# Kernel tuning notes

Hardware: AMD Instinct MI355X
Metric: run time of the kernel (lower is better)

Reference implementation:

```python
import jax, jax.numpy as jnp
import numpy as np

H = 2048      # hidden_size
NH = 32       # num attention heads
KVH = 8       # num kv heads
HD = 64       # head_dim
G = NH // KVH # kv groups (4)
EPS = 1e-6
THETA = 1000000.0


def _rms_norm(x, g):
    # normalize over last dim (head_dim)
    var = jnp.mean(jnp.square(x), axis=-1, keepdims=True)
    return x * jax.lax.rsqrt(var + EPS) * g


def _rope(seq_len, dtype):
    inv_freq = 1.0 / (THETA ** (jnp.arange(0, HD, 2, dtype=jnp.float32) / HD))
    pos = jnp.arange(seq_len, dtype=jnp.float32)
    freqs = pos[:, None] * inv_freq[None, :]          # [S, HD/2]
    emb = jnp.concatenate([freqs, freqs], axis=-1)    # [S, HD]
    return jnp.cos(emb).astype(dtype), jnp.sin(emb).astype(dtype)


def _rotate_half(x):
    x1, x2 = jnp.split(x, 2, axis=-1)
    return jnp.concatenate([-x2, x1], axis=-1)


def setup_inputs() -> dict:
    key = jax.random.key(0)
    ks = jax.random.split(key, 8)
    B, S = 1, 2048
    s = lambda fan_in: 1.0 / np.sqrt(fan_in)
    return {
        "hidden_states": jax.random.normal(ks[0], (B, S, H), jnp.float32),
        "Wq": jax.random.normal(ks[1], (H, NH * HD + NH), jnp.float32) * s(H),
        "Wk": jax.random.normal(ks[2], (H, KVH * HD), jnp.float32) * s(H),
        "Wv": jax.random.normal(ks[3], (H, KVH * HD), jnp.float32) * s(H),
        "Wo": jax.random.normal(ks[4], (NH * HD, H), jnp.float32) * s(NH * HD),
        "g_q": jnp.ones((HD,), jnp.float32),
        "g_k": jnp.ones((HD,), jnp.float32),
    }


def reference(hidden_states, Wq, Wk, Wv, Wo, g_q, g_k):
    B, S, _ = hidden_states.shape
    dtype = hidden_states.dtype

    qg = hidden_states @ Wq                              # [B,S,NH*HD+NH]
    k = hidden_states @ Wk                               # [B,S,KVH*HD]
    v = hidden_states @ Wv

    # headwise gate split, grouped per kv head (matches torch view/split)
    qg = qg.reshape(B, S, KVH, G * HD + G)
    q, gate = qg[..., : G * HD], qg[..., G * HD :]       # gate: [B,S,KVH,G]
    gate = gate.reshape(B, S, NH, 1)
    q = q.reshape(B, S, NH, HD).transpose(0, 2, 1, 3)    # [B,NH,S,HD]
    k = k.reshape(B, S, KVH, HD).transpose(0, 2, 1, 3)   # [B,KVH,S,HD]
    v = v.reshape(B, S, KVH, HD).transpose(0, 2, 1, 3)

    q = _rms_norm(q, g_q)
    k = _rms_norm(k, g_k)

    cos, sin = _rope(S, dtype)                           # [S,HD]
    cos, sin = cos[None, None], sin[None, None]
    q = q * cos + _rotate_half(q) * sin
    k = k * cos + _rotate_half(k) * sin

    # GQA: repeat kv heads
    k = jnp.repeat(k, G, axis=1)                         # [B,NH,S,HD]
    v = jnp.repeat(v, G, axis=1)

    # causal SDPA
    scale = 1.0 / np.sqrt(HD)
    scores = jnp.einsum("bhqd,bhkd->bhqk", q, k) * scale
    causal = jnp.tril(jnp.ones((S, S), bool))
    scores = jnp.where(causal[None, None], scores, jnp.finfo(dtype).min)
    probs = jax.nn.softmax(scores, axis=-1)
    attn = jnp.einsum("bhqk,bhkd->bhqd", probs, v)       # [B,NH,S,HD]

    attn = attn.transpose(0, 2, 1, 3)                    # [B,S,NH,HD]
    attn = attn * jax.nn.sigmoid(gate)
    attn = attn.reshape(B, S, NH * HD)
    return attn @ Wo
```

## Files before the change

### kernel.cpp

```cpp
#include <hip/hip_runtime.h>
#include <hip/hip_bf16.h>

#define SLEN 2048
#define HDIM 2048
#define NHEAD 32
#define KVHEAD 8
#define HEADD 64
#define NTOT 3104
#define NPAD 3200

typedef short bh8 __attribute__((ext_vector_type(8)));
typedef float f32x4 __attribute__((ext_vector_type(4)));

#define QSCALE 0.1803368801111204f

__device__ __forceinline__ unsigned short f2bf(float f) {
    union { float f; unsigned int u; } v; v.f = f;
    unsigned int u = v.u;
    return (unsigned short)((u + 0x7fffu + ((u >> 16) & 1u)) >> 16);
}

__device__ __forceinline__ unsigned int cvtpk_bf16(float lo, float hi) {
    unsigned int r;
    asm("v_cvt_pk_bf16_f32 %0, %1, %2" : "=v"(r) : "v"(lo), "v"(hi));
    return r;
}

__device__ __forceinline__ void gl_lds16(const unsigned short* g, unsigned short* l) {
    __builtin_amdgcn_global_load_lds(
        (const __attribute__((address_space(1))) unsigned int*)g,
        (__attribute__((address_space(3))) unsigned int*)l, 16, 0, 0);
}

__global__ void cast_x_k(const float* __restrict__ src, unsigned short* __restrict__ dst, int n) {
    int i = blockIdx.x * blockDim.x + threadIdx.x;
    int base = i * 4;
    if (base < n) {
        float4 f = *(const float4*)(src + base);
        ushort4 o;
        o.x = f2bf(f.x); o.y = f2bf(f.y); o.z = f2bf(f.z); o.w = f2bf(f.w);
        *(ushort4*)(dst + base) = o;
    }
}

__global__ void pack_wt_k(const float* __restrict__ Wq, const float* __restrict__ Wk,
                          const float* __restrict__ Wv, unsigned short* __restrict__ Wt) {
    __shared__ float tile[32][33];
    int n0 = blockIdx.x * 32, k0 = blockIdx.y * 32;
    int t = threadIdx.x;
    for (int i = 0; i < 4; i++) {
        int idx = i * 256 + t;
        int kr = idx >> 5, nc = idx & 31;
        int n = n0 + nc, k = k0 + kr;
        float val = 0.f;
        if (n < 2048)       { int h = n >> 6, d = n & 63; val = Wq[(size_t)k * 2080 + (h >> 2) * 260 + (h & 3) * 64 + d]; }
        else if (n < 2080)  { int h = n - 2048;           val = Wq[(size_t)k * 2080 + (h >> 2) * 260 + 256 + (h & 3)]; }
        else if (n < 2592)  { val = Wk[(size_t)k * 512 + (n - 2080)]; }
        else if (n < 3104)  { val = Wv[(size_t)k * 512 + (n - 2592)]; }
        tile[kr][nc] = val;
    }
    __syncthreads();
    for (int i = 0; i < 4; i++) {
        int idx = i * 256 + t;
        int nr = idx >> 5, kc = idx & 31;
        Wt[(size_t)(n0 + nr) * HDIM + (k0 + kc)] = f2bf(tile[kc][nr]);
    }
}

__global__ void pack_wot_k(const float* __restrict__ Wo, unsigned short* __restrict__ Wt) {
    __shared__ float tile[32][33];
    int n0 = blockIdx.x * 32, k0 = blockIdx.y * 32;
    int t = threadIdx.x;
    for (int i = 0; i < 4; i++) {
        int idx = i * 256 + t;
        int kr = idx >> 5, nc = idx & 31;
        tile[kr][nc] = Wo[(size_t)(k0 + kr) * 2048 + (n0 + nc)];
    }
    __syncthreads();
    for (int i = 0; i < 4; i++) {
        int idx = i * 256 + t;
        int nr = idx >> 5, kc = idx & 31;
        Wt[(size_t)(n0 + nr) * 2048 + (k0 + kc)] = f2bf(tile[kc][nr]);
    }
}

__global__ __launch_bounds__(256) void gemm_nt_k(const unsigned short* __restrict__ A,
                                                 const unsigned short* __restrict__ Bt,
                                                 float* __restrict__ C,
                                                 int K, int ldc) {
    __shared__ unsigned short As[3][128 * 32];
    __shared__ unsigned short Bs[3][128 * 32];
    int d = blockIdx.y * gridDim.x + blockIdx.x;
    int nwg = gridDim.x * gridDim.y;
    int cpx = nwg >> 3;
    int swz = (d & 7) * cpx + (d >> 3);
    int m0 = (swz % gridDim.x) * 128, n0 = (swz / gridDim.x) * 128;
    int t = threadIdx.x;
    int w = t >> 6, l = t & 63;
    int wm = (w >> 1) * 64, wn = (w & 1) * 64;
    int lrow = l & 15, lc = l >> 4;
    int rsw = (lrow >> 1) & 3;
    int srowA = w * 32 + (l >> 2);
    int scol = ((l & 3) ^ ((l >> 3) & 3)) * 8;

    f32x4 acc[4][4];
    #pragma unroll
    for (int i = 0; i < 4; i++)
        #pragma unroll
        for (int j = 0; j < 4; j++)
            acc[i][j] = {0.f, 0.f, 0.f, 0.f};

    const unsigned short* ga = &A[(size_t)(m0 + srowA) * K + scol];
    const unsigned short* gb = &Bt[(size_t)(n0 + srowA) * K + scol];
    int nst = K >> 5;

#define STAGE_NT(s, b) do { \
        const unsigned short* ga0 = ga + (size_t)(s) * 32; \
        const unsigned short* gb0 = gb + (size_t)(s) * 32; \
        gl_lds16(ga0,                  &As[b][(w * 2 + 0) * 512]); \
        gl_lds16(ga0 + 16 * (size_t)K, &As[b][(w * 2 + 1) * 512]); \
        gl_lds16(gb0,                  &Bs[b][(w * 2 + 0) * 512]); \
        gl_lds16(gb0 + 16 * (size_t)K, &Bs[b][(w * 2 + 1) * 512]); \
    } while (0)

    STAGE_NT(0, 0);
    STAGE_NT(1, 1);
    int rd = 0, wr = 2;
    for (int s = 0; s < nst; s++) {
        if (s + 1 < nst) asm volatile("s_waitcnt vmcnt(4)\n\ts_barrier" ::: "memory");
        else             asm volatile("s_waitcnt vmcnt(0)\n\ts_barrier" ::: "memory");
        if (s + 2 < nst) STAGE_NT(s + 2, wr);
        bh8 af[4], bb[4];
        #pragma unroll
        for (int i = 0; i < 4; i++) {
            af[i] = *(const bh8*)(&As[rd][(wm + i * 16 + lrow) * 32 + ((lc ^ rsw) * 8)]);
            bb[i] = *(const bh8*)(&Bs[rd][(wn + i * 16 + lrow) * 32 + ((lc ^ rsw) * 8)]);
        }
        #pragma unroll
        for (int i = 0; i < 4; i++)
            #pragma unroll
            for (int j = 0; j < 4; j++)
                acc[i][j] = __builtin_amdgcn_mfma_f32_16x16x32_bf16(af[i], bb[j], acc[i][j], 0, 0, 0);
        rd = (rd == 2) ? 0 : rd + 1;
        wr = (wr == 2) ? 0 : wr + 1;
    }
#undef STAGE_NT
    int col = l & 15, rbase = (l >> 4) * 4;
    for (int i = 0; i < 4; i++)
        for (int j = 0; j < 4; j++)
            #pragma unroll
            for (int r = 0; r < 4; r++)
                C[(size_t)(m0 + wm + i * 16 + rbase + r) * ldc + (n0 + wn + j * 16 + col)] = acc[i][j][r];
}

__global__ __launch_bounds__(256) void gemm_nt64_k(const unsigned short* __restrict__ A,
                                                   const unsigned short* __restrict__ Bt,
                                                   float* __restrict__ C) {
    const int K = 2048, ldc = 2048;
    __shared__ unsigned short As[3][64 * 32];
    __shared__ unsigned short Bs[3][128 * 32];
    int d = blockIdx.x;
    int swz = (d & 7) * 64 + (d >> 3);
    int m0 = (swz & 31) * 64, n0 = (swz >> 5) * 128;
    int t = threadIdx.x;
    int w = t >> 6, l = t & 63;
    int wm = (w >> 1) * 32, wn = (w & 1) * 64;
    int lrow = l & 15, lc = l >> 4;
    int rsw = (lrow >> 1) & 3;
    int scol = ((l & 3) ^ ((l >> 3) & 3)) * 8;

    f32x4 acc[2][4];
    #pragma unroll
    for (int i = 0; i < 2; i++)
        #pragma unroll
        for (int j = 0; j < 4; j++)
            acc[i][j] = {0.f, 0.f, 0.f, 0.f};

    const unsigned short* ga = &A[(size_t)(m0 + w * 16 + (l >> 2)) * K + scol];
    const unsigned short* gb = &Bt[(size_t)(n0 + w * 32 + (l >> 2)) * K + scol];
    const int nst = K >> 5;

#define STAGE_NT64(s, b) do { \
        gl_lds16(ga + (size_t)(s) * 32,                  &As[b][w * 512]); \
        gl_lds16(gb + (size_t)(s) * 32,                  &Bs[b][(w * 2 + 0) * 512]); \
        gl_lds16(gb + (size_t)(s) * 32 + 16 * (size_t)K, &Bs[b][(w * 2 + 1) * 512]); \
    } while (0)

    STAGE_NT64(0, 0);
    STAGE_NT64(1, 1);
    int rd = 0, wr = 2;
    for (int s = 0; s < nst; s++) {
        if (s + 1 < nst) asm volatile("s_waitcnt vmcnt(3)\n\ts_barrier" ::: "memory");
        else             asm volatile("s_waitcnt vmcnt(0)\n\ts_barrier" ::: "memory");
        if (s + 2 < nst) STAGE_NT64(s + 2, wr);
        bh8 af[2], bb[4];
        #pragma unroll
        for (int i = 0; i < 2; i++)
            af[i] = *(const bh8*)(&As[rd][(wm + i * 16 + lrow) * 32 + ((lc ^ rsw) * 8)]);
        #pragma unroll
        for (int j = 0; j < 4; j++)
            bb[j] = *(const bh8*)(&Bs[rd][(wn + j * 16 + lrow) * 32 + ((lc ^ rsw) * 8)]);
        #pragma unroll
        for (int i = 0; i < 2; i++)
            #pragma unroll
            for (int j = 0; j < 4; j++)
                acc[i][j] = __builtin_amdgcn_mfma_f32_16x16x32_bf16(af[i], bb[j], acc[i][j], 0, 0, 0);
        rd = (rd == 2) ? 0 : rd + 1;
        wr = (wr == 2) ? 0 : wr + 1;
    }
#undef STAGE_NT64
    int col = l & 15, rbase = (l >> 4) * 4;
    for (int i = 0; i < 2; i++)
        for (int j = 0; j < 4; j++)
            #pragma unroll
            for (int r = 0; r < 4; r++)
                C[(size_t)(m0 + wm + i * 16 + rbase + r) * ldc + (n0 + wn + j * 16 + col)] = acc[i][j][r];
}

__global__ void norm_rope_k(const float* __restrict__ QKVG, unsigned short* __restrict__ Qr,
                            unsigned short* __restrict__ Kr,
                            const float* __restrict__ g_q, const float* __restrict__ g_k) {
    int wid = blockIdx.x * (blockDim.x >> 6) + (threadIdx.x >> 6);
    int lane = threadIdx.x & 63;
    int type, s, hh;
    if (wid < SLEN * NHEAD) { type = 0; s = wid >> 5; hh = wid & 31; }
    else                    { int r = wid - SLEN * NHEAD; type = 1; s = r >> 3; hh = r & 7; }
    int col = (type == 0) ? hh * 64 + lane : 2080 + hh * 64 + lane;
    float x = QKVG[(size_t)s * NPAD + col];
    float sq = x * x;
    #pragma unroll
    for (int off = 32; off; off >>= 1) sq += __shfl_xor(sq, off);
    float inv = rsqrtf(sq * (1.f / 64.f) + 1e-6f);
    float g = (type == 0 ? g_q : g_k)[lane];
    float xn = x * inv * g;
    float xp = __shfl_xor(xn, 32);
    float xr = (lane < 32) ? -xp : xp;
    int i = lane & 31;
    float invf = __expf(-(float)i * (0.03125f * 13.815510557964274f));
    float ang = (float)s * invf;
    float c = cosf(ang), sn = sinf(ang);
    float r = xn * c + xr * sn;
    if (type == 0) Qr[((size_t)hh * SLEN + s) * 64 + lane] = f2bf(r * QSCALE);
    else           Kr[((size_t)hh * SLEN + s) * 64 + lane] = f2bf(r);
}

__global__ void vt_k(const float* __restrict__ QKVG, unsigned short* __restrict__ Vt) {
    __shared__ float tile[64][65];
    int s0 = blockIdx.x * 64, hh = blockIdx.y;
    int t = threadIdx.x;
    #pragma unroll
    for (int i = 0; i < 4; i++) {
        int idx = i * 256 + t;
        int sr = idx >> 4, c4 = (idx & 15) * 4;
        float4 f = *(const float4*)(&QKVG[(size_t)(s0 + sr) * NPAD + 2592 + hh * 64 + c4]);
        tile[sr][c4] = f.x; tile[sr][c4 + 1] = f.y; tile[sr][c4 + 2] = f.z; tile[sr][c4 + 3] = f.w;
    }
    __syncthreads();
    #pragma unroll
    for (int i = 0; i < 4; i++) {
        int idx = i * 256 + t;
        int dr = idx >> 4, c4 = (idx & 15) * 4;
        int hb = c4 >> 5, f = (c4 >> 4) & 1, g = (c4 >> 2) & 3;
        int p = (hb * 4 + g) * 8 + f * 4;
        ushort4 o;
        o.x = f2bf(tile[c4][dr]); o.y = f2bf(tile[c4 + 1][dr]);
        o.z = f2bf(tile[c4 + 2][dr]); o.w = f2bf(tile[c4 + 3][dr]);
        *(ushort4*)(&Vt[((size_t)hh * 64 + dr) * SLEN + s0 + p]) = o;
    }
}

__global__ void gate_sig_k(const float* __restrict__ QKVG, float* __restrict__ gate) {
    int i = blockIdx.x * 256 + threadIdx.x;
    int s = i >> 5, h = i & 31;
    float x = QKVG[(size_t)s * NPAD + 2048 + h];
    gate[i] = 1.f / (1.f + __expf(-x));
}

__global__ __launch_bounds__(256) void attn_k(const unsigned short* __restrict__ Qr,
                                              const unsigned short* __restrict__ Kr,
                                              const unsigned short* __restrict__ Vt,
                                              const float* __restrict__ gate,
                                              unsigned short* __restrict__ attn) {
    __shared__ unsigned short Kls[3][64 * 64];
    __shared__ unsigned short Vls[3][64 * 64];
    int d = blockIdx.y * gridDim.x + blockIdx.x;
    int kvh = d & 7;
    int j8 = d >> 3;
    int h = kvh * 4 + (j8 >> 4);
    int xp = j8 & 15;
    int t = threadIdx.x, w = t >> 6, l = t & 63;
    int ql = l & 15, g = l >> 4;
    const float NEGINF = -__builtin_inff();

    const unsigned short* Kh = Kr + (size_t)kvh * SLEN * 64;
    const unsigned short* Vh = Vt + (size_t)kvh * 64 * SLEN;
    const unsigned short* Qh = Qr + (size_t)h * SLEN * 64;
    int lk = g * 8;
    int r8 = l >> 3, c8 = l & 7;
    int cs = 8 * (c8 ^ r8);
    int R0 = w * 16, R1 = w * 16 + 8;
    int rdswz = (ql & 7) << 4;

    for (int half = 0; half < 2; half++) {
        int qt = half ? 31 - xp : xp;
        int q0 = qt * 64;
        int qrow = q0 + w * 16 + ql;

        bh8 qa0 = *(const bh8*)(Qh + (size_t)qrow * 64 + lk);
        bh8 qa1 = *(const bh8*)(Qh + (size_t)qrow * 64 + 32 + lk);

        f32x4 o[4];
        #pragma unroll
        for (int i = 0; i < 4; i++) o[i] = {0.f, 0.f, 0.f, 0.f};
        float m2 = NEGINF, lsum = 0.f;

        int ntiles = qt + 1;
        {
            gl_lds16(&Kh[(size_t)(0 + R0 + r8) * 64 + cs], &Kls[0][R0 * 64]);
            gl_lds16(&Kh[(size_t)(0 + R1 + r8) * 64 + cs], &Kls[0][R1 * 64]);
            gl_lds16(&Vh[(size_t)(R0 + r8) * SLEN + 0 + cs], &Vls[0][R0 * 64]);
            gl_lds16(&Vh[(size_t)(R1 + r8) * SLEN + 0 + cs], &Vls[0][R1 * 64]);
        }
        if (ntiles > 1) {
            gl_lds16(&Kh[(size_t)(64 + R0 + r8) * 64 + cs], &Kls[1][R0 * 64]);
            gl_lds16(&Kh[(size_t)(64 + R1 + r8) * 64 + cs], &Kls[1][R1 * 64]);
            gl_lds16(&Vh[(size_t)(R0 + r8) * SLEN + 64 + cs], &Vls[1][R0 * 64]);
            gl_lds16(&Vh[(size_t)(R1 + r8) * SLEN + 64 + cs], &Vls[1][R1 * 64]);
        }
        int rd = 0, wr = 2;

        for (int ti = 0; ti < ntiles; ti++) {
            if (ti + 1 < ntiles) asm volatile("s_waitcnt vmcnt(4)\n\ts_barrier" ::: "memory");
            else                 asm volatile("s_waitcnt vmcnt(0)\n\ts_barrier" ::: "memory");
            if (ti + 2 < ntiles) {
                int kv1 = (ti + 2) * 64;
                gl_lds16(&Kh[(size_t)(kv1 + R0 + r8) * 64 + cs], &Kls[wr][R0 * 64]);
                gl_lds16(&Kh[(size_t)(kv1 + R1 + r8) * 64 + cs], &Kls[wr][R1 * 64]);
                gl_lds16(&Vh[(size_t)(R0 + r8) * SLEN + kv1 + cs], &Vls[wr][R0 * 64]);
                gl_lds16(&Vh[(size_t)(R1 + r8) * SLEN + kv1 + cs], &Vls[wr][R1 * 64]);
            }
            const unsigned short* Kb = &Kls[rd][0];
            const unsigned short* Vb = &Vls[rd][0];
            int kv0 = ti * 64;
            f32x4 sct[4];
            #pragma unroll
            for (int nt = 0; nt < 4; nt++) {
                int rb = (nt * 16 + ql) * 128;
                bh8 kb0 = *(const bh8*)(&Kb[(rb + ((g * 16) ^ rdswz)) >> 1]);
                bh8 kb1 = *(const bh8*)(&Kb[(rb + ((64 + g * 16) ^ rdswz)) >> 1]);
                f32x4 a = {0.f, 0.f, 0.f, 0.f};
                a = __builtin_amdgcn_mfma_f32_16x16x32_bf16(kb0, qa0, a, 0, 0, 0);
                a = __builtin_amdgcn_mfma_f32_16x16x32_bf16(kb1, qa1, a, 0, 0, 0);
                sct[nt] = a;
            }
            if (ti == qt) {
                #pragma unroll
                for (int nt = 0; nt < 4; nt++)
                    #pragma unroll
                    for (int j = 0; j < 4; j++) {
                        int key = kv0 + nt * 16 + 4 * g + j;
                        if (key > qrow) sct[nt][j] = NEGINF;
                    }
            }
            float mt0 = fmaxf(fmaxf(sct[0][0], sct[0][1]), fmaxf(sct[0][2], sct[0][3]));
            float mt1 = fmaxf(fmaxf(sct[1][0], sct[1][1]), fmaxf(sct[1][2], sct[1][3]));
            float mt2 = fmaxf(fmaxf(sct[2][0], sct[2][1]), fmaxf(sct[2][2], sct[2][3]));
            float mt3 = fmaxf(fmaxf(sct[3][0], sct[3][1]), fmaxf(sct[3][2], sct[3][3]));
            float mt = fmaxf(fmaxf(mt0, mt1), fmaxf(mt2, mt3));
            mt = fmaxf(mt, __shfl_xor(mt, 16));
            mt = fmaxf(mt, __shfl_xor(mt, 32));
            if (!__all(mt - m2 <= 8.f)) {
                float mnew = fmaxf(m2, mt);
                float resc = __builtin_amdgcn_exp2f(m2 - mnew);
                m2 = mnew;
                lsum *= resc;
                float rf[4];
                #pragma unroll
                for (int j = 0; j < 4; j++) rf[j] = __shfl(resc, 4 * g + j);
                #pragma unroll
                for (int nt = 0; nt < 4; nt++) {
                    f32x4 oo = o[nt];
                    #pragma unroll
                    for (int j = 0; j < 4; j++) oo[j] *= rf[j];
                    o[nt] = oo;
                }
            }
            float ps = 0.f;
            #pragma unroll
            for (int nt = 0; nt < 4; nt++)
                #pragma unroll
                for (int j = 0; j < 4; j++) {
                    float p = __builtin_amdgcn_exp2f(sct[nt][j] - m2);
                    sct[nt][j] = p;
                    ps += p;
                }
            ps += __shfl_xor(ps, 16);
            ps += __shfl_xor(ps, 32);
            lsum += ps;
            union { unsigned int u[4]; bh8 v; } pa0, pa1;
            pa0.u[0] = cvtpk_bf16(sct[0][0], sct[0][1]);
            pa0.u[1] = cvtpk_bf16(sct[0][2], sct[0][3]);
            pa0.u[2] = cvtpk_bf16(sct[1][0], sct[1][1]);
            pa0.u[3] = cvtpk_bf16(sct[1][2], sct[1][3]);
            pa1.u[0] = cvtpk_bf16(sct[2][0], sct[2][1]);
            pa1.u[1] = cvtpk_bf16(sct[2][2], sct[2][3]);
            pa1.u[2] = cvtpk_bf16(sct[3][0], sct[3][1]);
            pa1.u[3] = cvtpk_bf16(sct[3][2], sct[3][3]);
            #pragma unroll
            for (int nt = 0; nt < 4; nt++) {
                int rb = (nt * 16 + ql) * 128;
                bh8 vb0 = *(const bh8*)(&Vb[(rb + ((g * 16) ^ rdswz)) >> 1]);
                bh8 vb1 = *(const bh8*)(&Vb[(rb + ((64 + g * 16) ^ rdswz)) >> 1]);
                o[nt] = __builtin_amdgcn_mfma_f32_16x16x32_bf16(pa0.v, vb0, o[nt], 0, 0, 0);
                o[nt] = __builtin_amdgcn_mfma_f32_16x16x32_bf16(pa1.v, vb1, o[nt], 0, 0, 0);
            }
            rd = (rd == 2) ? 0 : rd + 1;
            wr = (wr == 2) ? 0 : wr + 1;
        }
        asm volatile("s_barrier" ::: "memory");

        float gf[4];
        #pragma unroll
        for (int j = 0; j < 4; j++) {
            float ls = __shfl(lsum, 4 * g + j);
            int row = q0 + w * 16 + 4 * g + j;
            gf[j] = gate[row * 32 + h] / ls;
        }
        #pragma unroll
        for (int j = 0; j < 4; j++) {
            int row = q0 + w * 16 + 4 * g + j;
            #pragma unroll
            for (int nt = 0; nt < 4; nt++)
                attn[(size_t)row * 2048 + h * 64 + nt * 16 + ql] = f2bf(o[nt][j] * gf[j]);
        }
    }
}

extern "C" void kernel_launch(void* const* d_in, const int* in_sizes, int n_in,
                              void* d_out, int out_size, void* d_ws, size_t ws_size,
                              hipStream_t stream) {
    const float* hidden = (const float*)d_in[0];
    const float* Wq = (const float*)d_in[1];
    const float* Wk = (const float*)d_in[2];
    const float* Wv = (const float*)d_in[3];
    const float* Wo = (const float*)d_in[4];
    const float* gq = (const float*)d_in[5];
    const float* gk = (const float*)d_in[6];
    float* out = (float*)d_out;
    char* ws = (char*)d_ws;

    unsigned short* X    = (unsigned short*)(ws + 0);
    unsigned short* Wt   = (unsigned short*)(ws + 8388608);
    float*          QKVG = (float*)(ws + 21495808);
    unsigned short* Qr   = (unsigned short*)(ws + 47710208);
    unsigned short* Kr   = (unsigned short*)(ws + 56098816);
    unsigned short* Vt   = (unsigned short*)(ws + 58195968);
    float*          gate = (float*)(ws + 60293120);
    unsigned short* attn = (unsigned short*)(ws + 60555264);
    unsigned short* Wot  = (unsigned short*)(ws + 68943872);

    cast_x_k<<<dim3(4096), dim3(256), 0, stream>>>(hidden, X, SLEN * HDIM);
    pack_wt_k<<<dim3(100, 64), dim3(256), 0, stream>>>(Wq, Wk, Wv, Wt);
    pack_wot_k<<<dim3(64, 64), dim3(256), 0, stream>>>(Wo, Wot);
    gemm_nt_k<<<dim3(16, 25), dim3(256), 0, stream>>>(X, Wt, QKVG, HDIM, NPAD);
    norm_rope_k<<<dim3(20480), dim3(256), 0, stream>>>(QKVG, Qr, Kr, gq, gk);
    vt_k<<<dim3(32, 8), dim3(256), 0, stream>>>(QKVG, Vt);
    gate_sig_k<<<dim3(256), dim3(256), 0, stream>>>(QKVG, gate);
    attn_k<<<dim3(16, 32), dim3(256), 0, stream>>>(Qr, Kr, Vt, gate, attn);
    gemm_nt64_k<<<dim3(512), dim3(256), 0, stream>>>(attn, Wot, out);
}
```

Measured before the change: 170.1 us.

## Reuse 64x128 GEMM for QKV projection, split attention blocks, add MFMA priority

The QKV projection now uses the 64x128-tile GEMM kernel with a generic swizzle (800 workgroups) instead of the 128x128 kernel, giving more workgroups to fill the CUs. The attention kernel drops its paired-half causal balancing and launches one workgroup per (head, q-tile), ordered longest-first, over 1024 blocks. s_setprio is raised around MFMA sections in both the GEMM and attention kernels to favour matrix work among co-resident waves. The risks are lower per-block data reuse in the smaller GEMM tile and load imbalance in the tail of the attention grid.

```diff
diff --git a/kernel.cpp b/kernel.cpp
--- a/kernel.cpp
+++ b/kernel.cpp
@@ -84,84 +84,18 @@
     }
 }
 
-__global__ __launch_bounds__(256) void gemm_nt_k(const unsigned short* __restrict__ A,
-                                                 const unsigned short* __restrict__ Bt,
-                                                 float* __restrict__ C,
-                                                 int K, int ldc) {
-    __shared__ unsigned short As[3][128 * 32];
-    __shared__ unsigned short Bs[3][128 * 32];
-    int d = blockIdx.y * gridDim.x + blockIdx.x;
-    int nwg = gridDim.x * gridDim.y;
-    int cpx = nwg >> 3;
-    int swz = (d & 7) * cpx + (d >> 3);
-    int m0 = (swz % gridDim.x) * 128, n0 = (swz / gridDim.x) * 128;
-    int t = threadIdx.x;
-    int w = t >> 6, l = t & 63;
-    int wm = (w >> 1) * 64, wn = (w & 1) * 64;
-    int lrow = l & 15, lc = l >> 4;
-    int rsw = (lrow >> 1) & 3;
-    int srowA = w * 32 + (l >> 2);
-    int scol = ((l & 3) ^ ((l >> 3) & 3)) * 8;
-
-    f32x4 acc[4][4];
-    #pragma unroll
-    for (int i = 0; i < 4; i++)
-        #pragma unroll
-        for (int j = 0; j < 4; j++)
-            acc[i][j] = {0.f, 0.f, 0.f, 0.f};
-
-    const unsigned short* ga = &A[(size_t)(m0 + srowA) * K + scol];
-    const unsigned short* gb = &Bt[(size_t)(n0 + srowA) * K + scol];
-    int nst = K >> 5;
-
-#define STAGE_NT(s, b) do { \
-        const unsigned short* ga0 = ga + (size_t)(s) * 32; \
-        const unsigned short* gb0 = gb + (size_t)(s) * 32; \
-        gl_lds16(ga0,                  &As[b][(w * 2 + 0) * 512]); \
-        gl_lds16(ga0 + 16 * (size_t)K, &As[b][(w * 2 + 1) * 512]); \
-        gl_lds16(gb0,                  &Bs[b][(w * 2 + 0) * 512]); \
-        gl_lds16(gb0 + 16 * (size_t)K, &Bs[b][(w * 2 + 1) * 512]); \
-    } while (0)
-
-    STAGE_NT(0, 0);
-    STAGE_NT(1, 1);
-    int rd = 0, wr = 2;
-    for (int s = 0; s < nst; s++) {
-        if (s + 1 < nst) asm volatile("s_waitcnt vmcnt(4)\n\ts_barrier" ::: "memory");
-        else             asm volatile("s_waitcnt vmcnt(0)\n\ts_barrier" ::: "memory");
-        if (s + 2 < nst) STAGE_NT(s + 2, wr);
-        bh8 af[4], bb[4];
-        #pragma unroll
-        for (int i = 0; i < 4; i++) {
-            af[i] = *(const bh8*)(&As[rd][(wm + i * 16 + lrow) * 32 + ((lc ^ rsw) * 8)]);
-            bb[i] = *(const bh8*)(&Bs[rd][(wn + i * 16 + lrow) * 32 + ((lc ^ rsw) * 8)]);
-        }
-        #pragma unroll
-        for (int i = 0; i < 4; i++)
-            #pragma unroll
-            for (int j = 0; j < 4; j++)
-                acc[i][j] = __builtin_amdgcn_mfma_f32_16x16x32_bf16(af[i], bb[j], acc[i][j], 0, 0, 0);
-        rd = (rd == 2) ? 0 : rd + 1;
-        wr = (wr == 2) ? 0 : wr + 1;
-    }
-#undef STAGE_NT
-    int col = l & 15, rbase = (l >> 4) * 4;
-    for (int i = 0; i < 4; i++)
-        for (int j = 0; j < 4; j++)
-            #pragma unroll
-            for (int r = 0; r < 4; r++)
-                C[(size_t)(m0 + wm + i * 16 + rbase + r) * ldc + (n0 + wn + j * 16 + col)] = acc[i][j][r];
-}
-
 __global__ __launch_bounds__(256) void gemm_nt64_k(const unsigned short* __restrict__ A,
                                                    const unsigned short* __restrict__ Bt,
-                                                   float* __restrict__ C) {
-    const int K = 2048, ldc = 2048;
+                                                   float* __restrict__ C,
+                                                   int ldc, int mtiles) {
+    const int K = 2048;
     __shared__ unsigned short As[3][64 * 32];
     __shared__ unsigned short Bs[3][128 * 32];
     int d = blockIdx.x;
-    int swz = (d & 7) * 64 + (d >> 3);
-    int m0 = (swz & 31) * 64, n0 = (swz >> 5) * 128;
+    int nwg = gridDim.x;
+    int cpx = nwg >> 3;
+    int swz = (d & 7) * cpx + (d >> 3);
+    int m0 = (swz % mtiles) * 64, n0 = (swz / mtiles) * 128;
     int t = threadIdx.x;
     int w = t >> 6, l = t & 63;
     int wm = (w >> 1) * 32, wn = (w & 1) * 64;
@@ -200,11 +134,13 @@
         #pragma unroll
         for (int j = 0; j < 4; j++)
             bb[j] = *(const bh8*)(&Bs[rd][(wn + j * 16 + lrow) * 32 + ((lc ^ rsw) * 8)]);
+        __builtin_amdgcn_s_setprio(1);
         #pragma unroll
         for (int i = 0; i < 2; i++)
             #pragma unroll
             for (int j = 0; j < 4; j++)
                 acc[i][j] = __builtin_amdgcn_mfma_f32_16x16x32_bf16(af[i], bb[j], acc[i][j], 0, 0, 0);
+        __builtin_amdgcn_s_setprio(0);
         rd = (rd == 2) ? 0 : rd + 1;
         wr = (wr == 2) ? 0 : wr + 1;
     }
@@ -283,11 +219,10 @@
                                               unsigned short* __restrict__ attn) {
     __shared__ unsigned short Kls[3][64 * 64];
     __shared__ unsigned short Vls[3][64 * 64];
-    int d = blockIdx.y * gridDim.x + blockIdx.x;
+    int d = blockIdx.x;
     int kvh = d & 7;
-    int j8 = d >> 3;
-    int h = kvh * 4 + (j8 >> 4);
-    int xp = j8 & 15;
+    int h = kvh * 4 + ((d >> 3) & 3);
+    int qt = 31 - (d >> 5);
     int t = threadIdx.x, w = t >> 6, l = t & 63;
     int ql = l & 15, g = l >> 4;
     const float NEGINF = -__builtin_inff();
@@ -301,138 +236,138 @@
     int R0 = w * 16, R1 = w * 16 + 8;
     int rdswz = (ql & 7) << 4;
 
-    for (int half = 0; half < 2; half++) {
-        int qt = half ? 31 - xp : xp;
-        int q0 = qt * 64;
-        int qrow = q0 + w * 16 + ql;
-
-        bh8 qa0 = *(const bh8*)(Qh + (size_t)qrow * 64 + lk);
-        bh8 qa1 = *(const bh8*)(Qh + (size_t)qrow * 64 + 32 + lk);
-
-        f32x4 o[4];
-        #pragma unroll
-        for (int i = 0; i < 4; i++) o[i] = {0.f, 0.f, 0.f, 0.f};
-        float m2 = NEGINF, lsum = 0.f;
-
-        int ntiles = qt + 1;
-        {
-            gl_lds16(&Kh[(size_t)(0 + R0 + r8) * 64 + cs], &Kls[0][R0 * 64]);
-            gl_lds16(&Kh[(size_t)(0 + R1 + r8) * 64 + cs], &Kls[0][R1 * 64]);
-            gl_lds16(&Vh[(size_t)(R0 + r8) * SLEN + 0 + cs], &Vls[0][R0 * 64]);
-            gl_lds16(&Vh[(size_t)(R1 + r8) * SLEN + 0 + cs], &Vls[0][R1 * 64]);
+    int q0 = qt * 64;
+    int qrow = q0 + w * 16 + ql;
+
+    bh8 qa0 = *(const bh8*)(Qh + (size_t)qrow * 64 + lk);
+    bh8 qa1 = *(const bh8*)(Qh + (size_t)qrow * 64 + 32 + lk);
+
+    f32x4 o[4];
+    #pragma unroll
+    for (int i = 0; i < 4; i++) o[i] = {0.f, 0.f, 0.f, 0.f};
+    float m2 = NEGINF, lsum = 0.f;
+
+    int ntiles = qt + 1;
+    {
+        gl_lds16(&Kh[(size_t)(0 + R0 + r8) * 64 + cs], &Kls[0][R0 * 64]);
+        gl_lds16(&Kh[(size_t)(0 + R1 + r8) * 64 + cs], &Kls[0][R1 * 64]);
+        gl_lds16(&Vh[(size_t)(R0 + r8) * SLEN + 0 + cs], &Vls[0][R0 * 64]);
+        gl_lds16(&Vh[(size_t)(R1 + r8) * SLEN + 0 + cs], &Vls[0][R1 * 64]);
+    }
+    if (ntiles > 1) {
+        gl_lds16(&Kh[(size_t)(64 + R0 + r8) * 64 + cs], &Kls[1][R0 * 64]);
+        gl_lds16(&Kh[(size_t)(64 + R1 + r8) * 64 + cs], &Kls[1][R1 * 64]);
+        gl_lds16(&Vh[(size_t)(R0 + r8) * SLEN + 64 + cs], &Vls[1][R0 * 64]);
+        gl_lds16(&Vh[(size_t)(R1 + r8) * SLEN + 64 + cs], &Vls[1][R1 * 64]);
+    }
+    int rd = 0, wr = 2;
+
+    for (int ti = 0; ti < ntiles; ti++) {
+        if (ti + 1 < ntiles) asm volatile("s_waitcnt vmcnt(4)\n\ts_barrier" ::: "memory");
+        else                 asm volatile("s_waitcnt vmcnt(0)\n\ts_barrier" ::: "memory");
+        if (ti + 2 < ntiles) {
+            int kv1 = (ti + 2) * 64;
+            gl_lds16(&Kh[(size_t)(kv1 + R0 + r8) * 64 + cs], &Kls[wr][R0 * 64]);
+            gl_lds16(&Kh[(size_t)(kv1 + R1 + r8) * 64 + cs], &Kls[wr][R1 * 64]);
+            gl_lds16(&Vh[(size_t)(R0 + r8) * SLEN + kv1 + cs], &Vls[wr][R0 * 64]);
+            gl_lds16(&Vh[(size_t)(R1 + r8) * SLEN + kv1 + cs], &Vls[wr][R1 * 64]);
         }
-        if (ntiles > 1) {
-            gl_lds16(&Kh[(size_t)(64 + R0 + r8) * 64 + cs], &Kls[1][R0 * 64]);
-            gl_lds16(&Kh[(size_t)(64 + R1 + r8) * 64 + cs], &Kls[1][R1 * 64]);
-            gl_lds16(&Vh[(size_t)(R0 + r8) * SLEN + 64 + cs], &Vls[1][R0 * 64]);
-            gl_lds16(&Vh[(size_t)(R1 + r8) * SLEN + 64 + cs], &Vls[1][R1 * 64]);
+        const unsigned short* Kb = &Kls[rd][0];
+        const unsigned short* Vb = &Vls[rd][0];
+        int kv0 = ti * 64;
+        f32x4 sct[4];
+        __builtin_amdgcn_s_setprio(1);
+        #pragma unroll
+        for (int nt = 0; nt < 4; nt++) {
+            int rb = (nt * 16 + ql) * 128;
+            bh8 kb0 = *(const bh8*)(&Kb[(rb + ((g * 16) ^ rdswz)) >> 1]);
+            bh8 kb1 = *(const bh8*)(&Kb[(rb + ((64 + g * 16) ^ rdswz)) >> 1]);
+            f32x4 a = {0.f, 0.f, 0.f, 0.f};
+            a = __builtin_amdgcn_mfma_f32_16x16x32_bf16(kb0, qa0, a, 0, 0, 0);
+            a = __builtin_amdgcn_mfma_f32_16x16x32_bf16(kb1, qa1, a, 0, 0, 0);
+            sct[nt] = a;
         }
-        int rd = 0, wr = 2;
-
-        for (int ti = 0; ti < ntiles; ti++) {
-            if (ti + 1 < ntiles) asm volatile("s_waitcnt vmcnt(4)\n\ts_barrier" ::: "memory");
-            else                 asm volatile("s_waitcnt vmcnt(0)\n\ts_barrier" ::: "memory");
-            if (ti + 2 < ntiles) {
-                int kv1 = (ti + 2) * 64;
-                gl_lds16(&Kh[(size_t)(kv1 + R0 + r8) * 64 + cs], &Kls[wr][R0 * 64]);
-                gl_lds16(&Kh[(size_t)(kv1 + R1 + r8) * 64 + cs], &Kls[wr][R1 * 64]);
-                gl_lds16(&Vh[(size_t)(R0 + r8) * SLEN + kv1 + cs], &Vls[wr][R0 * 64]);
-                gl_lds16(&Vh[(size_t)(R1 + r8) * SLEN + kv1 + cs], &Vls[wr][R1 * 64]);
-            }
-            const unsigned short* Kb = &Kls[rd][0];
-            const unsigned short* Vb = &Vls[rd][0];
-            int kv0 = ti * 64;
-            f32x4 sct[4];
-            #pragma unroll
-            for (int nt = 0; nt < 4; nt++) {
-                int rb = (nt * 16 + ql) * 128;
-                bh8 kb0 = *(const bh8*)(&Kb[(rb + ((g * 16) ^ rdswz)) >> 1]);
-                bh8 kb1 = *(const bh8*)(&Kb[(rb + ((64 + g * 16) ^ rdswz)) >> 1]);
-                f32x4 a = {0.f, 0.f, 0.f, 0.f};
-                a = __builtin_amdgcn_mfma_f32_16x16x32_bf16(kb0, qa0, a, 0, 0, 0);
-                a = __builtin_amdgcn_mfma_f32_16x16x32_bf16(kb1, qa1, a, 0, 0, 0);
-                sct[nt] = a;
-            }
-            if (ti == qt) {
-                #pragma unroll
-                for (int nt = 0; nt < 4; nt++)
-                    #pragma unroll
-                    for (int j = 0; j < 4; j++) {
-                        int key = kv0 + nt * 16 + 4 * g + j;
-                        if (key > qrow) sct[nt][j] = NEGINF;
-                    }
-            }
-            float mt0 = fmaxf(fmaxf(sct[0][0], sct[0][1]), fmaxf(sct[0][2], sct[0][3]));
-            float mt1 = fmaxf(fmaxf(sct[1][0], sct[1][1]), fmaxf(sct[1][2], sct[1][3]));
-            float mt2 = fmaxf(fmaxf(sct[2][0], sct[2][1]), fmaxf(sct[2][2], sct[2][3]));
-            float mt3 = fmaxf(fmaxf(sct[3][0], sct[3][1]), fmaxf(sct[3][2], sct[3][3]));
-            float mt = fmaxf(fmaxf(mt0, mt1), fmaxf(mt2, mt3));
-            mt = fmaxf(mt, __shfl_xor(mt, 16));
-            mt = fmaxf(mt, __shfl_xor(mt, 32));
-            if (!__all(mt - m2 <= 8.f)) {
-                float mnew = fmaxf(m2, mt);
-                float resc = __builtin_amdgcn_exp2f(m2 - mnew);
-                m2 = mnew;
-                lsum *= resc;
-                float rf[4];
-                #pragma unroll
-                for (int j = 0; j < 4; j++) rf[j] = __shfl(resc, 4 * g + j);
-                #pragma unroll
-                for (int nt = 0; nt < 4; nt++) {
-                    f32x4 oo = o[nt];
-                    #pragma unroll
-                    for (int j = 0; j < 4; j++) oo[j] *= rf[j];
-                    o[nt] = oo;
-                }
-            }
-            float ps = 0.f;
+        __builtin_amdgcn_s_setprio(0);
+        if (ti == qt) {
             #pragma unroll
             for (int nt = 0; nt < 4; nt++)
                 #pragma unroll
                 for (int j = 0; j < 4; j++) {
-                    float p = __builtin_amdgcn_exp2f(sct[nt][j] - m2);
-                    sct[nt][j] = p;
-                    ps += p;
+                    int key = kv0 + nt * 16 + 4 * g + j;
+                    if (key > qrow) sct[nt][j] = NEGINF;
                 }
-            ps += __shfl_xor(ps, 16);
-            ps += __shfl_xor(ps, 32);
-            lsum += ps;
-            union { unsigned int u[4]; bh8 v; } pa0, pa1;
-            pa0.u[0] = cvtpk_bf16(sct[0][0], sct[0][1]);
-            pa0.u[1] = cvtpk_bf16(sct[0][2], sct[0][3]);
-            pa0.u[2] = cvtpk_bf16(sct[1][0], sct[1][1]);
-            pa0.u[3] = cvtpk_bf16(sct[1][2], sct[1][3]);
-            pa1.u[0] = cvtpk_bf16(sct[2][0], sct[2][1]);
-            pa1.u[1] = cvtpk_bf16(sct[2][2], sct[2][3]);
-            pa1.u[2] = cvtpk_bf16(sct[3][0], sct[3][1]);
-            pa1.u[3] = cvtpk_bf16(sct[3][2], sct[3][3]);
+        }
+        float mt0 = fmaxf(fmaxf(sct[0][0], sct[0][1]), fmaxf(sct[0][2], sct[0][3]));
+        float mt1 = fmaxf(fmaxf(sct[1][0], sct[1][1]), fmaxf(sct[1][2], sct[1][3]));
+        float mt2 = fmaxf(fmaxf(sct[2][0], sct[2][1]), fmaxf(sct[2][2], sct[2][3]));
+        float mt3 = fmaxf(fmaxf(sct[3][0], sct[3][1]), fmaxf(sct[3][2], sct[3][3]));
+        float mt = fmaxf(fmaxf(mt0, mt1), fmaxf(mt2, mt3));
+        mt = fmaxf(mt, __shfl_xor(mt, 16));
+        mt = fmaxf(mt, __shfl_xor(mt, 32));
+        if (!__all(mt - m2 <= 8.f)) {
+            float mnew = fmaxf(m2, mt);
+            float resc = __builtin_amdgcn_exp2f(m2 - mnew);
+            m2 = mnew;
+            lsum *= resc;
+            float rf[4];
+            #pragma unroll
+            for (int j = 0; j < 4; j++) rf[j] = __shfl(resc, 4 * g + j);
             #pragma unroll
             for (int nt = 0; nt < 4; nt++) {
-                int rb = (nt * 16 + ql) * 128;
-                bh8 vb0 = *(const bh8*)(&Vb[(rb + ((g * 16) ^ rdswz)) >> 1]);
-                bh8 vb1 = *(const bh8*)(&Vb[(rb + ((64 + g * 16) ^ rdswz)) >> 1]);
-                o[nt] = __builtin_amdgcn_mfma_f32_16x16x32_bf16(pa0.v, vb0, o[nt], 0, 0, 0);
-                o[nt] = __builtin_amdgcn_mfma_f32_16x16x32_bf16(pa1.v, vb1, o[nt], 0, 0, 0);
+                f32x4 oo = o[nt];
+                #pragma unroll
+                for (int j = 0; j < 4; j++) oo[j] *= rf[j];
+                o[nt] = oo;
             }
-            rd = (rd == 2) ? 0 : rd + 1;
-            wr = (wr == 2) ? 0 : wr + 1;
         }
-        asm volatile("s_barrier" ::: "memory");
-
-        float gf[4];
-        #pragma unroll
-        for (int j = 0; j < 4; j++) {
-            float ls = __shfl(lsum, 4 * g + j);
-            int row = q0 + w * 16 + 4 * g + j;
-            gf[j] = gate[row * 32 + h] / ls;
+        float ps = 0.f;
+        #pragma unroll
+        for (int nt = 0; nt < 4; nt++)
+            #pragma unroll
+            for (int j = 0; j < 4; j++) {
+                float p = __builtin_amdgcn_exp2f(sct[nt][j] - m2);
+                sct[nt][j] = p;
+                ps += p;
+            }
+        ps += __shfl_xor(ps, 16);
+        ps += __shfl_xor(ps, 32);
+        lsum += ps;
+        union { unsigned int u[4]; bh8 v; } pa0, pa1;
+        pa0.u[0] = cvtpk_bf16(sct[0][0], sct[0][1]);
+        pa0.u[1] = cvtpk_bf16(sct[0][2], sct[0][3]);
+        pa0.u[2] = cvtpk_bf16(sct[1][0], sct[1][1]);
+        pa0.u[3] = cvtpk_bf16(sct[1][2], sct[1][3]);
+        pa1.u[0] = cvtpk_bf16(sct[2][0], sct[2][1]);
+        pa1.u[1] = cvtpk_bf16(sct[2][2], sct[2][3]);
+        pa1.u[2] = cvtpk_bf16(sct[3][0], sct[3][1]);
+        pa1.u[3] = cvtpk_bf16(sct[3][2], sct[3][3]);
+        __builtin_amdgcn_s_setprio(1);
+        #pragma unroll
+        for (int nt = 0; nt < 4; nt++) {
+            int rb = (nt * 16 + ql) * 128;
+            bh8 vb0 = *(const bh8*)(&Vb[(rb + ((g * 16) ^ rdswz)) >> 1]);
+            bh8 vb1 = *(const bh8*)(&Vb[(rb + ((64 + g * 16) ^ rdswz)) >> 1]);
+            o[nt] = __builtin_amdgcn_mfma_f32_16x16x32_bf16(pa0.v, vb0, o[nt], 0, 0, 0);
+            o[nt] = __builtin_amdgcn_mfma_f32_16x16x32_bf16(pa1.v, vb1, o[nt], 0, 0, 0);
         }
-        #pragma unroll
-        for (int j = 0; j < 4; j++) {
-            int row = q0 + w * 16 + 4 * g + j;
-            #pragma unroll
-            for (int nt = 0; nt < 4; nt++)
-                attn[(size_t)row * 2048 + h * 64 + nt * 16 + ql] = f2bf(o[nt][j] * gf[j]);
-        }
+        __builtin_amdgcn_s_setprio(0);
+        rd = (rd == 2) ? 0 : rd + 1;
+        wr = (wr == 2) ? 0 : wr + 1;
+    }
+
+    float gf[4];
+    #pragma unroll
+    for (int j = 0; j < 4; j++) {
+        float ls = __shfl(lsum, 4 * g + j);
+        int row = q0 + w * 16 + 4 * g + j;
+        gf[j] = gate[row * 32 + h] / ls;
+    }
+    #pragma unroll
+    for (int j = 0; j < 4; j++) {
+        int row = q0 + w * 16 + 4 * g + j;
+        #pragma unroll
+        for (int nt = 0; nt < 4; nt++)
+            attn[(size_t)row * 2048 + h * 64 + nt * 16 + ql] = f2bf(o[nt][j] * gf[j]);
     }
 }
 
@@ -462,10 +397,10 @@
     cast_x_k<<<dim3(4096), dim3(256), 0, stream>>>(hidden, X, SLEN * HDIM);
     pack_wt_k<<<dim3(100, 64), dim3(256), 0, stream>>>(Wq, Wk, Wv, Wt);
     pack_wot_k<<<dim3(64, 64), dim3(256), 0, stream>>>(Wo, Wot);
-    gemm_nt_k<<<dim3(16, 25), dim3(256), 0, stream>>>(X, Wt, QKVG, HDIM, NPAD);
+    gemm_nt64_k<<<dim3(800), dim3(256), 0, stream>>>(X, Wt, QKVG, NPAD, 32);
     norm_rope_k<<<dim3(20480), dim3(256), 0, stream>>>(QKVG, Qr, Kr, gq, gk);
     vt_k<<<dim3(32, 8), dim3(256), 0, stream>>>(QKVG, Vt);
     gate_sig_k<<<dim3(256), dim3(256), 0, stream>>>(QKVG, gate);
-    attn_k<<<dim3(16, 32), dim3(256), 0, stream>>>(Qr, Kr, Vt, gate, attn);
-    gemm_nt64_k<<<dim3(512), dim3(256), 0, stream>>>(attn, Wot, out);
-}
+    attn_k<<<dim3(1024), dim3(256), 0, stream>>>(Qr, Kr, Vt, gate, attn);
+    gemm_nt64_k<<<dim3(512), dim3(256), 0, stream>>>(attn, Wot, out, 2048, 32);
+}
```

New measurement: 180.1 us. 1.06x slower.
